# Performance work log

Hardware: AMD Instinct MI355X
Metric: run time of the kernel (lower is better)

Reference implementation:

```python
import jax, jax.numpy as jnp
import numpy as np
import math

B = 1048576
BG_RES = 512
NUM_LEVELS = 2
POWER = 4
MIPNOISE = 0.5
INIT_VAL = -2.0


def cube_face_uv(v):
    # v: [N,3] direction vectors. OpenGL cubemap face convention
    # (faces: 0:+x 1:-x 2:+y 3:-y 4:+z 5:-z), as used by nvdiffrast 'cube'.
    x, y, z = v[:, 0], v[:, 1], v[:, 2]
    ax, ay, az = jnp.abs(x), jnp.abs(y), jnp.abs(z)
    is_x = (ax >= ay) & (ax >= az)
    is_y = (~is_x) & (ay >= az)
    face = jnp.where(is_x, jnp.where(x >= 0, 0, 1),
                     jnp.where(is_y, jnp.where(y >= 0, 2, 3),
                               jnp.where(z >= 0, 4, 5))).astype(jnp.int32)
    ma = jnp.where(is_x, ax, jnp.where(is_y, ay, az))
    sc = jnp.where(is_x, jnp.where(x >= 0, -z, z),
                   jnp.where(is_y, x, jnp.where(z >= 0, x, -x)))
    tc = jnp.where(is_x, -y, jnp.where(is_y, jnp.where(y >= 0, z, -z), -y))
    u = 0.5 * (sc / ma + 1.0)
    t = 0.5 * (tc / ma + 1.0)
    return face, u, t


def build_pyramid(tex):
    # tex: [6,R,R,3] -> list of 2x2 box-filtered mips down to 1x1 (nvdiffrast style)
    levels = [tex]
    t = tex
    while t.shape[1] > 1:
        R = t.shape[1]
        t = t.reshape(6, R // 2, 2, R // 2, 2, 3).mean(axis=(2, 4))
        levels.append(t)
    return levels


def bilinear(tex, face, u, v):
    # tex: [6,R,R,3]; face/u/v: [N]. Clamp-to-edge bilinear per selected face.
    R = tex.shape[1]
    x = u * R - 0.5
    y = v * R - 0.5
    x0f = jnp.floor(x); y0f = jnp.floor(y)
    fx = (x - x0f)[:, None]; fy = (y - y0f)[:, None]
    x0 = jnp.clip(x0f.astype(jnp.int32), 0, R - 1)
    y0 = jnp.clip(y0f.astype(jnp.int32), 0, R - 1)
    x1 = jnp.clip(x0f.astype(jnp.int32) + 1, 0, R - 1)
    y1 = jnp.clip(y0f.astype(jnp.int32) + 1, 0, R - 1)
    flat = tex.reshape(6 * R * R, 3)
    base = face * (R * R)
    g00 = flat[base + y0 * R + x0]
    g01 = flat[base + y0 * R + x1]
    g10 = flat[base + y1 * R + x0]
    g11 = flat[base + y1 * R + x1]
    return ((1 - fx) * (1 - fy) * g00 + fx * (1 - fy) * g01 +
            (1 - fx) * fy * g10 + fx * fy * g11)


def sample_cubemap(tex6, face, u, v, mip):
    # trilinear: bilinear in two adjacent mips, lerp by fractional mip level
    levels = build_pyramid(tex6)
    lmax = float(len(levels) - 1)
    m = jnp.clip(mip, 0.0, lmax)
    out = jnp.zeros((face.shape[0], 3), tex6.dtype)
    for l, t in enumerate(levels):
        wl = jnp.clip(1.0 - jnp.abs(m - l), 0.0, 1.0)  # (1-f)/f trilinear weights
        out = out + wl[:, None] * bilinear(t, face, u, v)
    return out


def setup_inputs() -> dict:
    key = jax.random.key(0)
    k1, k2, k3, k4, k5 = jax.random.split(key, 5)
    viewdirs = jax.random.normal(k1, (B, 3), dtype=jnp.float32)
    viewdirs = viewdirs / jnp.linalg.norm(viewdirs, axis=-1, keepdims=True)
    saSample = jax.random.normal(k2, (B,), dtype=jnp.float32)
    noise_u = jax.random.uniform(k3, (B,), dtype=jnp.float32)
    # parameters (init_val*ones/(num_levels-i) in torch; perturbed for nontrivial grads)
    bg_mat0 = (INIT_VAL * jnp.ones((1, 6, 128, 128, 3), jnp.float32)
               + 0.1 * jax.random.normal(k4, (1, 6, 128, 128, 3), jnp.float32))
    bg_mat1 = (INIT_VAL / 2.0 * jnp.ones((1, 6, 512, 512, 3), jnp.float32)
               + 0.1 * jax.random.normal(k5, (1, 6, 512, 512, 3), jnp.float32))
    return {
        "viewdirs": viewdirs,
        "saSample": saSample,
        "noise_u": noise_u,
        "bg_mat0": bg_mat0,
        "bg_mat1": bg_mat1,
        "brightness": jnp.asarray(0.0, jnp.float32),
        "mul": jnp.asarray(1.0, jnp.float32),
        "mipbias": jnp.asarray(0.5, jnp.float32),
    }


def reference(viewdirs, saSample, noise_u, bg_mat0, bg_mat1, brightness, mul, mipbias):
    h = w = BG_RES  # from bg_mats[-1]
    # sa2mip
    distortion = 1.0 / jnp.max(jnp.abs(viewdirs), axis=-1)  # 1/||u||_inf
    saTexel = distortion / h / w
    miplevel = ((saSample - jnp.log(saTexel)) / math.log(POWER) / 2.0
                + mipbias + MIPNOISE * noise_u)
    miplevel = jnp.maximum(miplevel, 0.0)

    face, u, t = cube_face_uv(viewdirs)
    sumemb = sample_cubemap(bg_mat0[0], face, u, t, miplevel)  # mip 1 (128)
    sumemb = sumemb + sample_cubemap(bg_mat1[0], face, u, t, miplevel)  # mip 0 (512)

    # activation == 'identity' branch: exp(x).clip(0.01, 1000)
    img = jnp.clip(jnp.exp(jnp.clip(brightness, -1.0, 2.0) + mul * sumemb), 0.01, 1000.0)
    return img
```

## Files before the change

### kernel.cpp

```cpp
#include <hip/hip_runtime.h>
#include <hip/hip_bf16.h>
#include <math.h>


#define NPYR1 1572858
#define NPYR0 98298

__device__ __constant__ int OFFS0[7] = {0, 73728, 92160, 96768, 97920, 98208, 98280};
__device__ __constant__ int OFFS1[9] = {0, 1179648, 1474560, 1548288, 1566720,
                                        1571328, 1572480, 1572768, 1572840};
static const int H_OFFS0[7] = {0, 73728, 92160, 96768, 97920, 98208, 98280};
static const int H_OFFS1[9] = {0, 1179648, 1474560, 1548288, 1566720,
                               1571328, 1572480, 1572768, 1572840};

struct PyrArgs {
    const float* src;
    float* dst[5];
    int R;
    int tpf;
    int T;
    int nlev;
};

__global__ __launch_bounds__(256) void pyr_kernel(PyrArgs a0, PyrArgs a1, int split) {
    __shared__ float A[32 * 32 * 3];
    __shared__ float Bb[16 * 16 * 3];

    PyrArgs a = (blockIdx.x < (unsigned)split) ? a0 : a1;
    int bid = (blockIdx.x < (unsigned)split) ? blockIdx.x : blockIdx.x - split;

    const int tpf = a.tpf;
    const int face = bid / (tpf * tpf);
    const int tif = bid - face * tpf * tpf;
    const int ty = tif / tpf, tx = tif - (tif / tpf) * tpf;
    const int T = a.T, R = a.R;
    const int tid = threadIdx.x;
    const int baseY = ty * T, baseX = tx * T;

    const int total = T * T * 3;
    for (int idx = tid; idx < total; idx += 256) {
        int r = idx / (T * 3);
        int k = idx - r * (T * 3);
        A[r * (T * 3) + k] =
            a.src[((size_t)(face * R + baseY + r) * R + baseX) * 3 + k];
    }
    __syncthreads();

    float* cur = A;
    float* nxt = Bb;
    int curT = T;
    for (int l = 0; l < a.nlev; ++l) {
        const int nT = curT >> 1;
        const int Rg = R >> (l + 1);
        const int tb = T >> (l + 1);
        float* dst = a.dst[l];
        const int n = nT * nT * 3;
        for (int idx = tid; idx < n; idx += 256) {
            int c = idx % 3;
            int t2 = idx / 3;
            int ly = t2 / nT, lx = t2 - ly * nT;
            float s = 0.25f * (cur[((2 * ly) * curT + 2 * lx) * 3 + c] +
                               cur[((2 * ly) * curT + 2 * lx + 1) * 3 + c] +
                               cur[((2 * ly + 1) * curT + 2 * lx) * 3 + c] +
                               cur[((2 * ly + 1) * curT + 2 * lx + 1) * 3 + c]);
            nxt[(ly * nT + lx) * 3 + c] = s;
            dst[((size_t)(face * Rg + ty * tb + ly) * Rg + tx * tb + lx) * 3 + c] = s;
        }
        __syncthreads();
        float* tmp = cur; cur = nxt; nxt = tmp;
        curT = nT;
    }
}

__device__ __forceinline__ void bilin(const float* __restrict__ tex, int R,
                                      int face, float u, float v, float o[3]) {
    float xf = u * (float)R - 0.5f;
    float yf = v * (float)R - 0.5f;
    float x0f = floorf(xf), y0f = floorf(yf);
    float fx = xf - x0f, fy = yf - y0f;
    int xi = (int)x0f, yi = (int)y0f;
    int x0 = min(max(xi, 0), R - 1);
    int x1 = min(max(xi + 1, 0), R - 1);
    int y0 = min(max(yi, 0), R - 1);
    int y1 = min(max(yi + 1, 0), R - 1);
    const float* base = tex + (size_t)face * R * R * 3;
    const float* p00 = base + (y0 * R + x0) * 3;
    const float* p01 = base + (y0 * R + x1) * 3;
    const float* p10 = base + (y1 * R + x0) * 3;
    const float* p11 = base + (y1 * R + x1) * 3;
    float w00 = (1.f - fx) * (1.f - fy);
    float w01 = fx * (1.f - fy);
    float w10 = (1.f - fx) * fy;
    float w11 = fx * fy;
#pragma unroll
    for (int c = 0; c < 3; ++c)
        o[c] = w00 * p00[c] + w01 * p01[c] + w10 * p10[c] + w11 * p11[c];
}

__device__ __forceinline__ void sample_pyr(const float* __restrict__ base_tex,
                                           const float* __restrict__ pyr,
                                           const int* offs, int lmax, int R0,
                                           int face, float u, float v, float mip,
                                           float o[3]) {
    float m = fminf(fmaxf(mip, 0.f), (float)lmax);
    float l0f = floorf(m);
    int l0 = (int)l0f;
    float f = m - l0f;
    const float* t0 = (l0 == 0) ? base_tex : (pyr + offs[l0 - 1]);
    float c0[3];
    bilin(t0, R0 >> l0, face, u, v, c0);
    if (f > 0.f && l0 < lmax) {
        const float* t1 = pyr + offs[l0];
        float c1[3];
        bilin(t1, R0 >> (l0 + 1), face, u, v, c1);
        float w0 = 1.f - f;
#pragma unroll
        for (int c = 0; c < 3; ++c) o[c] = w0 * c0[c] + f * c1[c];
    } else {
#pragma unroll
        for (int c = 0; c < 3; ++c) o[c] = c0[c];
    }
}

__global__ __launch_bounds__(256) void sample_kernel(
    const float* __restrict__ vd, const float* __restrict__ sa,
    const float* __restrict__ nu, const float* __restrict__ tex0,
    const float* __restrict__ tex1, const float* __restrict__ sb,
    const float* __restrict__ sm, const float* __restrict__ smb,
    const float* __restrict__ pyr0, const float* __restrict__ pyr1,
    float* __restrict__ out, int n) {
    int i = blockIdx.x * 256 + threadIdx.x;
    if (i >= n) return;

    float x = vd[3 * i + 0];
    float y = vd[3 * i + 1];
    float z = vd[3 * i + 2];
    float ax = fabsf(x), ay = fabsf(y), az = fabsf(z);

    bool is_x = (ax >= ay) && (ax >= az);
    bool is_y = (!is_x) && (ay >= az);

    int face;
    float ma, sc, tc;
    if (is_x) {
        face = (x >= 0.f) ? 0 : 1;
        ma = ax;
        sc = (x >= 0.f) ? -z : z;
        tc = -y;
    } else if (is_y) {
        face = (y >= 0.f) ? 2 : 3;
        ma = ay;
        sc = x;
        tc = (y >= 0.f) ? z : -z;
    } else {
        face = (z >= 0.f) ? 4 : 5;
        ma = az;
        sc = (z >= 0.f) ? x : -x;
        tc = -y;
    }
    float u = 0.5f * (sc / ma + 1.f);
    float t = 0.5f * (tc / ma + 1.f);

    float distortion = 1.f / ma;
    float saTexel = distortion / 512.f / 512.f;
    float mip = (sa[i] - logf(saTexel)) / 1.3862943611198906f / 2.0f +
                smb[0] + 0.5f * nu[i];
    mip = fmaxf(mip, 0.f);

    float s0[3], s1[3];
    sample_pyr(tex0, pyr0, OFFS0, 7, 128, face, u, t, mip, s0);
    sample_pyr(tex1, pyr1, OFFS1, 9, 512, face, u, t, mip, s1);

    float b = fminf(fmaxf(sb[0], -1.f), 2.f);
    float mul = sm[0];
#pragma unroll
    for (int c = 0; c < 3; ++c) {
        float e = expf(b + mul * (s0[c] + s1[c]));
        out[3 * i + c] = fminf(fmaxf(e, 0.01f), 1000.f);
    }
}

extern "C" void kernel_launch(void* const* d_in, const int* in_sizes, int n_in,
                              void* d_out, int out_size, void* d_ws, size_t ws_size,
                              hipStream_t stream) {
    const float* vd = (const float*)d_in[0];
    const float* sa = (const float*)d_in[1];
    const float* nu = (const float*)d_in[2];
    const float* tex0 = (const float*)d_in[3];
    const float* tex1 = (const float*)d_in[4];
    const float* br = (const float*)d_in[5];
    const float* mu = (const float*)d_in[6];
    const float* mb = (const float*)d_in[7];
    float* out = (float*)d_out;

    float* pyr1 = (float*)d_ws;
    float* pyr0 = pyr1 + NPYR1;

    const int B = in_sizes[1];

    PyrArgs a0{}, a1{};
    a0.src = tex1; a0.R = 512; a0.tpf = 16; a0.T = 32; a0.nlev = 5;
    for (int l = 0; l < 5; ++l) a0.dst[l] = pyr1 + H_OFFS1[l];
    a1.src = tex0; a1.R = 128; a1.tpf = 4; a1.T = 32; a1.nlev = 5;
    for (int l = 0; l < 5; ++l) a1.dst[l] = pyr0 + H_OFFS0[l];
    int split1 = 6 * 16 * 16;
    int grid1 = split1 + 6 * 4 * 4;
    hipLaunchKernelGGL(pyr_kernel, dim3(grid1), dim3(256), 0, stream, a0, a1, split1);

    PyrArgs b0{}, b1{};
    b0.src = pyr1 + H_OFFS1[4]; b0.R = 16; b0.tpf = 1; b0.T = 16; b0.nlev = 4;
    for (int l = 0; l < 4; ++l) b0.dst[l] = pyr1 + H_OFFS1[5 + l];
    b1.src = pyr0 + H_OFFS0[4]; b1.R = 4; b1.tpf = 1; b1.T = 4; b1.nlev = 2;
    for (int l = 0; l < 2; ++l) b1.dst[l] = pyr0 + H_OFFS0[5 + l];
    hipLaunchKernelGGL(pyr_kernel, dim3(12), dim3(256), 0, stream, b0, b1, 6);

    int grid = (B + 255) / 256;
    hipLaunchKernelGGL(sample_kernel, dim3(grid), dim3(256), 0, stream,
                       vd, sa, nu, tex0, tex1, br, mu, mb, pyr0, pyr1, out, B);
}
```

Before: 138.3 us.

## Store mip pyramid levels as padded float4 RGBA for vectorized texel fetches

```diff
diff --git a/kernel.cpp b/kernel.cpp
--- a/kernel.cpp
+++ b/kernel.cpp
@@ -3,28 +3,28 @@
 #include <math.h>
 
 
-#define NPYR1 1572858
-#define NPYR0 98298
-
-__device__ __constant__ int OFFS0[7] = {0, 73728, 92160, 96768, 97920, 98208, 98280};
-__device__ __constant__ int OFFS1[9] = {0, 1179648, 1474560, 1548288, 1566720,
-                                        1571328, 1572480, 1572768, 1572840};
-static const int H_OFFS0[7] = {0, 73728, 92160, 96768, 97920, 98208, 98280};
-static const int H_OFFS1[9] = {0, 1179648, 1474560, 1548288, 1566720,
-                               1571328, 1572480, 1572768, 1572840};
+#define NPYR1_4 524286
+
+__device__ __constant__ int OFFS0[7] = {0, 24576, 30720, 32256, 32640, 32736, 32760};
+__device__ __constant__ int OFFS1[9] = {0, 393216, 491520, 516096, 522240,
+                                        523776, 524160, 524256, 524280};
+static const int H_OFFS0[7] = {0, 24576, 30720, 32256, 32640, 32736, 32760};
+static const int H_OFFS1[9] = {0, 393216, 491520, 516096, 522240,
+                               523776, 524160, 524256, 524280};
 
 struct PyrArgs {
-    const float* src;
-    float* dst[5];
+    const void* src;
+    float4* dst[5];
     int R;
     int tpf;
     int T;
     int nlev;
+    int rgba;
 };
 
 __global__ __launch_bounds__(256) void pyr_kernel(PyrArgs a0, PyrArgs a1, int split) {
-    __shared__ float A[32 * 32 * 3];
-    __shared__ float Bb[16 * 16 * 3];
+    __shared__ float4 A[32 * 32];
+    __shared__ float4 Bb[16 * 16];
 
     PyrArgs a = (blockIdx.x < (unsigned)split) ? a0 : a1;
     int bid = (blockIdx.x < (unsigned)split) ? blockIdx.x : blockIdx.x - split;
@@ -37,43 +37,77 @@
     const int tid = threadIdx.x;
     const int baseY = ty * T, baseX = tx * T;
 
-    const int total = T * T * 3;
-    for (int idx = tid; idx < total; idx += 256) {
-        int r = idx / (T * 3);
-        int k = idx - r * (T * 3);
-        A[r * (T * 3) + k] =
-            a.src[((size_t)(face * R + baseY + r) * R + baseX) * 3 + k];
+    const int total = T * T;
+    if (a.rgba) {
+        const float4* src = (const float4*)a.src;
+        for (int idx = tid; idx < total; idx += 256) {
+            int r = idx / T, c = idx - (idx / T) * T;
+            A[r * T + c] = src[(size_t)(face * R + baseY + r) * R + baseX + c];
+        }
+    } else {
+        const float* src = (const float*)a.src;
+        for (int idx = tid; idx < total; idx += 256) {
+            int r = idx / T, c = idx - (idx / T) * T;
+            const float* p = src + ((size_t)(face * R + baseY + r) * R + baseX + c) * 3;
+            A[r * T + c] = make_float4(p[0], p[1], p[2], 0.f);
+        }
     }
     __syncthreads();
 
-    float* cur = A;
-    float* nxt = Bb;
+    float4* cur = A;
+    float4* nxt = Bb;
     int curT = T;
     for (int l = 0; l < a.nlev; ++l) {
         const int nT = curT >> 1;
         const int Rg = R >> (l + 1);
         const int tb = T >> (l + 1);
-        float* dst = a.dst[l];
-        const int n = nT * nT * 3;
+        float4* dst = a.dst[l];
+        const int n = nT * nT;
         for (int idx = tid; idx < n; idx += 256) {
-            int c = idx % 3;
-            int t2 = idx / 3;
-            int ly = t2 / nT, lx = t2 - ly * nT;
-            float s = 0.25f * (cur[((2 * ly) * curT + 2 * lx) * 3 + c] +
-                               cur[((2 * ly) * curT + 2 * lx + 1) * 3 + c] +
-                               cur[((2 * ly + 1) * curT + 2 * lx) * 3 + c] +
-                               cur[((2 * ly + 1) * curT + 2 * lx + 1) * 3 + c]);
-            nxt[(ly * nT + lx) * 3 + c] = s;
-            dst[((size_t)(face * Rg + ty * tb + ly) * Rg + tx * tb + lx) * 3 + c] = s;
+            int ly = idx / nT, lx = idx - (idx / nT) * nT;
+            float4 q00 = cur[(2 * ly) * curT + 2 * lx];
+            float4 q01 = cur[(2 * ly) * curT + 2 * lx + 1];
+            float4 q10 = cur[(2 * ly + 1) * curT + 2 * lx];
+            float4 q11 = cur[(2 * ly + 1) * curT + 2 * lx + 1];
+            float4 s = make_float4(0.25f * (q00.x + q01.x + q10.x + q11.x),
+                                   0.25f * (q00.y + q01.y + q10.y + q11.y),
+                                   0.25f * (q00.z + q01.z + q10.z + q11.z), 0.f);
+            nxt[ly * nT + lx] = s;
+            dst[(size_t)(face * Rg + ty * tb + ly) * Rg + tx * tb + lx] = s;
         }
         __syncthreads();
-        float* tmp = cur; cur = nxt; nxt = tmp;
+        float4* tmp = cur; cur = nxt; nxt = tmp;
         curT = nT;
     }
 }
 
-__device__ __forceinline__ void bilin(const float* __restrict__ tex, int R,
-                                      int face, float u, float v, float o[3]) {
+__device__ __forceinline__ void bilin4(const float4* __restrict__ tex, int R,
+                                       int face, float u, float v, float o[3]) {
+    float xf = u * (float)R - 0.5f;
+    float yf = v * (float)R - 0.5f;
+    float x0f = floorf(xf), y0f = floorf(yf);
+    float fx = xf - x0f, fy = yf - y0f;
+    int xi = (int)x0f, yi = (int)y0f;
+    int x0 = min(max(xi, 0), R - 1);
+    int x1 = min(max(xi + 1, 0), R - 1);
+    int y0 = min(max(yi, 0), R - 1);
+    int y1 = min(max(yi + 1, 0), R - 1);
+    const float4* base = tex + (size_t)face * R * R;
+    float4 p00 = base[y0 * R + x0];
+    float4 p01 = base[y0 * R + x1];
+    float4 p10 = base[y1 * R + x0];
+    float4 p11 = base[y1 * R + x1];
+    float w00 = (1.f - fx) * (1.f - fy);
+    float w01 = fx * (1.f - fy);
+    float w10 = (1.f - fx) * fy;
+    float w11 = fx * fy;
+    o[0] = w00 * p00.x + w01 * p01.x + w10 * p10.x + w11 * p11.x;
+    o[1] = w00 * p00.y + w01 * p01.y + w10 * p10.y + w11 * p11.y;
+    o[2] = w00 * p00.z + w01 * p01.z + w10 * p10.z + w11 * p11.z;
+}
+
+__device__ __forceinline__ void bilin3(const float* __restrict__ tex, int R,
+                                       int face, float u, float v, float o[3]) {
     float xf = u * (float)R - 0.5f;
     float yf = v * (float)R - 0.5f;
     float x0f = floorf(xf), y0f = floorf(yf);
@@ -98,7 +132,7 @@
 }
 
 __device__ __forceinline__ void sample_pyr(const float* __restrict__ base_tex,
-                                           const float* __restrict__ pyr,
+                                           const float4* __restrict__ pyr,
                                            const int* offs, int lmax, int R0,
                                            int face, float u, float v, float mip,
                                            float o[3]) {
@@ -106,13 +140,14 @@
     float l0f = floorf(m);
     int l0 = (int)l0f;
     float f = m - l0f;
-    const float* t0 = (l0 == 0) ? base_tex : (pyr + offs[l0 - 1]);
     float c0[3];
-    bilin(t0, R0 >> l0, face, u, v, c0);
+    if (l0 == 0)
+        bilin3(base_tex, R0, face, u, v, c0);
+    else
+        bilin4(pyr + offs[l0 - 1], R0 >> l0, face, u, v, c0);
     if (f > 0.f && l0 < lmax) {
-        const float* t1 = pyr + offs[l0];
         float c1[3];
-        bilin(t1, R0 >> (l0 + 1), face, u, v, c1);
+        bilin4(pyr + offs[l0], R0 >> (l0 + 1), face, u, v, c1);
         float w0 = 1.f - f;
 #pragma unroll
         for (int c = 0; c < 3; ++c) o[c] = w0 * c0[c] + f * c1[c];
@@ -127,7 +162,7 @@
     const float* __restrict__ nu, const float* __restrict__ tex0,
     const float* __restrict__ tex1, const float* __restrict__ sb,
     const float* __restrict__ sm, const float* __restrict__ smb,
-    const float* __restrict__ pyr0, const float* __restrict__ pyr1,
+    const float4* __restrict__ pyr0, const float4* __restrict__ pyr1,
     float* __restrict__ out, int n) {
     int i = blockIdx.x * 256 + threadIdx.x;
     if (i >= n) return;
@@ -193,24 +228,24 @@
     const float* mb = (const float*)d_in[7];
     float* out = (float*)d_out;
 
-    float* pyr1 = (float*)d_ws;
-    float* pyr0 = pyr1 + NPYR1;
+    float4* pyr1 = (float4*)d_ws;
+    float4* pyr0 = pyr1 + NPYR1_4;
 
     const int B = in_sizes[1];
 
     PyrArgs a0{}, a1{};
-    a0.src = tex1; a0.R = 512; a0.tpf = 16; a0.T = 32; a0.nlev = 5;
+    a0.src = tex1; a0.R = 512; a0.tpf = 16; a0.T = 32; a0.nlev = 5; a0.rgba = 0;
     for (int l = 0; l < 5; ++l) a0.dst[l] = pyr1 + H_OFFS1[l];
-    a1.src = tex0; a1.R = 128; a1.tpf = 4; a1.T = 32; a1.nlev = 5;
+    a1.src = tex0; a1.R = 128; a1.tpf = 4; a1.T = 32; a1.nlev = 5; a1.rgba = 0;
     for (int l = 0; l < 5; ++l) a1.dst[l] = pyr0 + H_OFFS0[l];
     int split1 = 6 * 16 * 16;
     int grid1 = split1 + 6 * 4 * 4;
     hipLaunchKernelGGL(pyr_kernel, dim3(grid1), dim3(256), 0, stream, a0, a1, split1);
 
     PyrArgs b0{}, b1{};
-    b0.src = pyr1 + H_OFFS1[4]; b0.R = 16; b0.tpf = 1; b0.T = 16; b0.nlev = 4;
+    b0.src = pyr1 + H_OFFS1[4]; b0.R = 16; b0.tpf = 1; b0.T = 16; b0.nlev = 4; b0.rgba = 1;
     for (int l = 0; l < 4; ++l) b0.dst[l] = pyr1 + H_OFFS1[5 + l];
-    b1.src = pyr0 + H_OFFS0[4]; b1.R = 4; b1.tpf = 1; b1.T = 4; b1.nlev = 2;
+    b1.src = pyr0 + H_OFFS0[4]; b1.R = 4; b1.tpf = 1; b1.T = 4; b1.nlev = 2; b1.rgba = 1;
     for (int l = 0; l < 2; ++l) b1.dst[l] = pyr0 + H_OFFS0[5 + l];
     hipLaunchKernelGGL(pyr_kernel, dim3(12), dim3(256), 0, stream, b0, b1, 6);
 
```

Result: no change. 137.4 us (-0.6%).
